# Performance work log

Measured on AMD Instinct MI355X. Metric: run time of the kernel, lower is better.

## Reference

```python
import jax, jax.numpy as jnp
import numpy as np

N, D = 320, 64


def setup_inputs() -> dict:
    key = jax.random.key(0)
    k1, k2, k3, k4, k5 = jax.random.split(key, 5)
    x = jax.random.normal(k1, (N, D), dtype=jnp.float32)
    sigma = jax.random.uniform(k2, (), dtype=jnp.float32) + 0.5  # positive scalar bandwidth
    score = jax.random.normal(k3, (N, D), dtype=jnp.float32)
    v = jax.random.normal(k4, (N, D), dtype=jnp.float32)
    grad_v_score = jax.random.normal(k5, (N, D), dtype=jnp.float32)
    return {"x": x, "sigma": sigma, "score": score, "v": v, "grad_v_score": grad_v_score}


def reference(x, sigma, score, v, grad_v_score):
    d = x.shape[-1]
    # od[i, j, :] = x_i - x_j   (torch: x.unsqueeze(-2) - x.unsqueeze(-3))
    od = x[:, None, :] - x[None, :, :]              # [N, N, D]
    ods = od * od                                    # [N, N, D]
    gamma = 1.0 / (sigma * sigma + 1e-8)             # scalar
    gods = gamma * ods                               # [N, N, D]
    k_d = jnp.exp(-0.5 * gods)                       # [N, N, D]
    k = k_d.mean(-1)                                 # [N, N]
    k_xj = gamma * k_d * od / d                      # [N, N, D]
    k_xi = -k_xj                                     # [N, N, D]
    tr_k_xj_xi = (gamma * (1.0 - gods) * k_d).mean(-1)  # [N, N]

    # score^T k_xk_xi k_xi term: ((1-gods) * score_j * k_xi * gamma) @ k_d^T / D  -> [N, N, N]
    A = (1.0 - gods) * score[None, :, :] * k_xi * gamma  # [N, N, D]
    score_t_k_xk_xi_k_xi = jnp.einsum('ijd,ikd->ijk', A, k_d) / d  # [N, N, N]

    # tr(k_xj_xi^T k_xk_xi) term -> [N, N, N]
    dot = jnp.einsum('ijd,ikd->ijk', od, od)         # (x_i-x_j).(x_i-x_k)
    t1 = dot * dot * (4.0 * gamma * gamma)
    sq = ods.sum(-1)                                  # pairwise squared distance [N, N]
    t2 = -2.0 * gamma * (sq[:, :, None] + sq[:, None, :])
    tr_k_xj_xi_t_k_xk_xi = (t1 + t2 + d) * k[:, :, None] * k[:, None, :] * (4.0 * gamma * gamma)

    # v^T k_xj_xi grad_v_score term -> [N, N]
    a = jnp.einsum('id,ijd->ij', v, od)              # v_i . (x_i - x_j)
    b = jnp.einsum('id,ijd->ij', grad_v_score, od)   # gvs_i . (x_i - x_j)
    vdot = (v * grad_v_score).sum(-1)[:, None]       # [N, 1]
    v_t_k_xj_xi_grad_v_score = (-2.0 * gamma * a * b + vdot) * k * (2.0 * gamma)

    return (k, k_xj, k_xi, tr_k_xj_xi, score_t_k_xk_xi_k_xi,
            tr_k_xj_xi_t_k_xk_xi, v_t_k_xj_xi_grad_v_score)
```

## Files before the change

### kernel.cpp

```cpp
#include <hip/hip_runtime.h>

#define N 320
#define D 64

__global__ __launch_bounds__(256) void pair_kernel(
    const float* __restrict__ x, const float* __restrict__ sigma,
    const float* __restrict__ score, const float* __restrict__ v,
    const float* __restrict__ gvs,
    float* __restrict__ out_k, float* __restrict__ out_kxj,
    float* __restrict__ out_kxi, float* __restrict__ out_tr,
    float* __restrict__ out_vt,
    float* __restrict__ wsA, float* __restrict__ wsK,
    float* __restrict__ wsSQ, float* __restrict__ wsG)
{
    int lane = threadIdx.x & 63;
    int p = blockIdx.x * 4 + (threadIdx.x >> 6);
    int i = p / N;
    int j = p - i * N;

    float sg = sigma[0];
    float gamma = 1.0f / (sg * sg + 1e-8f);

    float xi = x[i * D + lane];
    float xj = x[j * D + lane];
    float od = xi - xj;
    float ods = od * od;
    float gods = gamma * ods;
    float kd = __expf(-0.5f * gods);

    float kxj = gamma * kd * od * (1.0f / D);
    size_t pd = (size_t)p * D + lane;
    out_kxj[pd] = kxj;
    out_kxi[pd] = -kxj;

    float sj = score[j * D + lane];
    float Aval = (1.0f - gods) * sj * (-kxj) * gamma;
    wsA[pd] = Aval;
    wsK[pd] = kd;

    float vi = v[i * D + lane];
    float gi = gvs[i * D + lane];

    float r0 = kd;
    float r1 = gamma * (1.0f - gods) * kd;
    float r2 = ods;
    float r3 = vi * od;
    float r4 = gi * od;
    float r5 = vi * gi;
    float r6 = xi * xj;

    #pragma unroll
    for (int off = 32; off > 0; off >>= 1) {
        r0 += __shfl_xor(r0, off, 64);
        r1 += __shfl_xor(r1, off, 64);
        r2 += __shfl_xor(r2, off, 64);
        r3 += __shfl_xor(r3, off, 64);
        r4 += __shfl_xor(r4, off, 64);
        r5 += __shfl_xor(r5, off, 64);
        r6 += __shfl_xor(r6, off, 64);
    }

    if (lane == 0) {
        float kmean = r0 * (1.0f / D);
        out_k[p]  = kmean;
        out_tr[p] = r1 * (1.0f / D);
        wsSQ[p]   = r2;
        wsG[p]    = r6;
        out_vt[p] = (-2.0f * gamma * r3 * r4 + r5) * kmean * 2.0f * gamma;
    }
}

__global__ __launch_bounds__(N) void t6_kernel(
    const float* __restrict__ sigma,
    const float* __restrict__ k, const float* __restrict__ wsSQ,
    const float* __restrict__ wsG, float* __restrict__ out6)
{
    int kk = threadIdx.x;
    int j = blockIdx.x;
    int i = blockIdx.y;

    float sg = sigma[0];
    float gamma = 1.0f / (sg * sg + 1e-8f);
    float g2 = 4.0f * gamma * gamma;

    float Gii  = wsG[i * N + i];
    float Gij  = wsG[i * N + j];
    float kij  = k[i * N + j];
    float sqij = wsSQ[i * N + j];

    float Gjk  = wsG[j * N + kk];
    float Gik  = wsG[i * N + kk];
    float kik  = k[i * N + kk];
    float sqik = wsSQ[i * N + kk];

    float dot = Gii - Gij - Gik + Gjk;
    float t1 = dot * dot * g2;
    float t2 = -2.0f * gamma * (sqij + sqik);
    out6[((size_t)i * N + j) * N + kk] = (t1 + t2 + (float)D) * kij * kik * g2;
}

__global__ __launch_bounds__(256) void s5_kernel(
    const float* __restrict__ wsA, const float* __restrict__ wsK,
    float* __restrict__ out5)
{
    __shared__ float Alds[64 * 64];
    __shared__ float Klds[64 * 64];

    int i   = blockIdx.z;
    int j0  = blockIdx.y * 64;
    int kk0 = blockIdx.x * 64;
    int tid = threadIdx.x;

    int cw = tid & 15, rw = tid >> 4;
    const float* Abase = wsA + (size_t)(i * N + j0) * D;
    const float* Kbase = wsK + (size_t)(i * N + kk0) * D;
    #pragma unroll
    for (int q = 0; q < 4; ++q) {
        int r = rw + 16 * q;
        float4 av = *(const float4*)(Abase + r * D + cw * 4);
        float4 kv = *(const float4*)(Kbase + r * D + cw * 4);
        int sc = ((cw ^ (r & 7)) << 2);
        *(float4*)&Alds[r * 64 + sc] = av;
        *(float4*)&Klds[r * 64 + sc] = kv;
    }
    __syncthreads();

    int tk = tid & 15, tj = tid >> 4;
    float acc[4][4];
    #pragma unroll
    for (int a = 0; a < 4; ++a)
        #pragma unroll
        for (int b = 0; b < 4; ++b) acc[a][b] = 0.0f;

    #pragma unroll
    for (int c = 0; c < 16; ++c) {
        float4 a4[4], k4[4];
        #pragma unroll
        for (int jj = 0; jj < 4; ++jj) {
            int r = tj + 16 * jj;
            a4[jj] = *(const float4*)&Alds[r * 64 + ((c ^ (r & 7)) << 2)];
        }
        #pragma unroll
        for (int kki = 0; kki < 4; ++kki) {
            int r = tk + 16 * kki;
            k4[kki] = *(const float4*)&Klds[r * 64 + ((c ^ (r & 7)) << 2)];
        }
        #pragma unroll
        for (int jj = 0; jj < 4; ++jj)
            #pragma unroll
            for (int kki = 0; kki < 4; ++kki)
                acc[jj][kki] += a4[jj].x * k4[kki].x + a4[jj].y * k4[kki].y
                              + a4[jj].z * k4[kki].z + a4[jj].w * k4[kki].w;
    }

    #pragma unroll
    for (int jj = 0; jj < 4; ++jj) {
        int j = j0 + tj + 16 * jj;
        #pragma unroll
        for (int kki = 0; kki < 4; ++kki) {
            int kk = kk0 + tk + 16 * kki;
            out5[((size_t)i * N + j) * N + kk] = acc[jj][kki] * (1.0f / D);
        }
    }
}

extern "C" void kernel_launch(void* const* d_in, const int* in_sizes, int n_in,
                              void* d_out, int out_size, void* d_ws, size_t ws_size,
                              hipStream_t stream) {
    const float* x     = (const float*)d_in[0];
    const float* sigma = (const float*)d_in[1];
    const float* score = (const float*)d_in[2];
    const float* v     = (const float*)d_in[3];
    const float* gvs   = (const float*)d_in[4];

    float* out = (float*)d_out;
    float* out_k   = out;
    float* out_kxj = out + 102400;
    float* out_kxi = out + 6656000;
    float* out_tr  = out + 13209600;
    float* out5    = out + 13312000;
    float* out6    = out + 46080000;
    float* out_vt  = out + 78848000;

    float* ws   = (float*)d_ws;
    float* wsA  = ws;
    float* wsK  = ws + 6553600;
    float* wsSQ = ws + 13107200;
    float* wsG  = ws + 13209600;

    pair_kernel<<<dim3(N * N / 4), dim3(256), 0, stream>>>(
        x, sigma, score, v, gvs,
        out_k, out_kxj, out_kxi, out_tr, out_vt, wsA, wsK, wsSQ, wsG);

    t6_kernel<<<dim3(N, N), dim3(N), 0, stream>>>(sigma, out_k, wsSQ, wsG, out6);

    s5_kernel<<<dim3(5, 5, N), dim3(256), 0, stream>>>(wsA, wsK, out5);
}
```

Baseline: 429.6 us.

## Fuse t6 into s5 tile kernel and recompute A/K tiles on the fly

Removes the wsA/wsK workspace tensors. The triple kernel now recomputes the A and k_d tiles from x and score directly in its LDS load phase, and writes the out6 term in the same block that writes out5. The pair kernel is also restructured so each thread handles four elements with float4 loads and stores, using 16-lane reductions. This cuts roughly 50 MB of workspace write and read traffic and one kernel launch, at the cost of redundant exp computations per tile and scattered output stores for out6.

```diff
diff --git a/kernel.cpp b/kernel.cpp
--- a/kernel.cpp
+++ b/kernel.cpp
@@ -10,47 +10,56 @@
     float* __restrict__ out_k, float* __restrict__ out_kxj,
     float* __restrict__ out_kxi, float* __restrict__ out_tr,
     float* __restrict__ out_vt,
-    float* __restrict__ wsA, float* __restrict__ wsK,
     float* __restrict__ wsSQ, float* __restrict__ wsG)
 {
-    int lane = threadIdx.x & 63;
-    int p = blockIdx.x * 4 + (threadIdx.x >> 6);
+    int tid = threadIdx.x;
+    int sub = tid & 15;
+    int p = blockIdx.x * 16 + (tid >> 4);
     int i = p / N;
     int j = p - i * N;
 
     float sg = sigma[0];
     float gamma = 1.0f / (sg * sg + 1e-8f);
 
-    float xi = x[i * D + lane];
-    float xj = x[j * D + lane];
-    float od = xi - xj;
-    float ods = od * od;
-    float gods = gamma * ods;
-    float kd = __expf(-0.5f * gods);
-
-    float kxj = gamma * kd * od * (1.0f / D);
-    size_t pd = (size_t)p * D + lane;
-    out_kxj[pd] = kxj;
-    out_kxi[pd] = -kxj;
-
-    float sj = score[j * D + lane];
-    float Aval = (1.0f - gods) * sj * (-kxj) * gamma;
-    wsA[pd] = Aval;
-    wsK[pd] = kd;
-
-    float vi = v[i * D + lane];
-    float gi = gvs[i * D + lane];
-
-    float r0 = kd;
-    float r1 = gamma * (1.0f - gods) * kd;
-    float r2 = ods;
-    float r3 = vi * od;
-    float r4 = gi * od;
-    float r5 = vi * gi;
-    float r6 = xi * xj;
-
-    #pragma unroll
-    for (int off = 32; off > 0; off >>= 1) {
+    float4 xi4 = *(const float4*)(x     + i * D + sub * 4);
+    float4 xj4 = *(const float4*)(x     + j * D + sub * 4);
+    float4 sj4 = *(const float4*)(score + j * D + sub * 4);
+    float4 vi4 = *(const float4*)(v     + i * D + sub * 4);
+    float4 gi4 = *(const float4*)(gvs   + i * D + sub * 4);
+    const float* xi = (const float*)&xi4;
+    const float* xj = (const float*)&xj4;
+    const float* vi = (const float*)&vi4;
+    const float* gi = (const float*)&gi4;
+
+    float4 kxj4, kxi4;
+    float* kxjp = (float*)&kxj4;
+    float* kxip = (float*)&kxi4;
+
+    float r0 = 0.f, r1 = 0.f, r2 = 0.f, r3 = 0.f, r4 = 0.f, r5 = 0.f, r6 = 0.f;
+    #pragma unroll
+    for (int c = 0; c < 4; ++c) {
+        float od   = xi[c] - xj[c];
+        float ods  = od * od;
+        float gods = gamma * ods;
+        float kd   = __expf(-0.5f * gods);
+        float kxj  = gamma * kd * od * (1.0f / D);
+        kxjp[c] = kxj;
+        kxip[c] = -kxj;
+        r0 += kd;
+        r1 += gamma * (1.0f - gods) * kd;
+        r2 += ods;
+        r3 += vi[c] * od;
+        r4 += gi[c] * od;
+        r5 += vi[c] * gi[c];
+        r6 += xi[c] * xj[c];
+    }
+
+    size_t pd = (size_t)p * D + sub * 4;
+    *(float4*)(out_kxj + pd) = kxj4;
+    *(float4*)(out_kxi + pd) = kxi4;
+
+    #pragma unroll
+    for (int off = 8; off > 0; off >>= 1) {
         r0 += __shfl_xor(r0, off, 64);
         r1 += __shfl_xor(r1, off, 64);
         r2 += __shfl_xor(r2, off, 64);
@@ -60,7 +69,7 @@
         r6 += __shfl_xor(r6, off, 64);
     }
 
-    if (lane == 0) {
+    if (sub == 0) {
         float kmean = r0 * (1.0f / D);
         out_k[p]  = kmean;
         out_tr[p] = r1 * (1.0f / D);
@@ -70,38 +79,12 @@
     }
 }
 
-__global__ __launch_bounds__(N) void t6_kernel(
-    const float* __restrict__ sigma,
-    const float* __restrict__ k, const float* __restrict__ wsSQ,
-    const float* __restrict__ wsG, float* __restrict__ out6)
-{
-    int kk = threadIdx.x;
-    int j = blockIdx.x;
-    int i = blockIdx.y;
-
-    float sg = sigma[0];
-    float gamma = 1.0f / (sg * sg + 1e-8f);
-    float g2 = 4.0f * gamma * gamma;
-
-    float Gii  = wsG[i * N + i];
-    float Gij  = wsG[i * N + j];
-    float kij  = k[i * N + j];
-    float sqij = wsSQ[i * N + j];
-
-    float Gjk  = wsG[j * N + kk];
-    float Gik  = wsG[i * N + kk];
-    float kik  = k[i * N + kk];
-    float sqik = wsSQ[i * N + kk];
-
-    float dot = Gii - Gij - Gik + Gjk;
-    float t1 = dot * dot * g2;
-    float t2 = -2.0f * gamma * (sqij + sqik);
-    out6[((size_t)i * N + j) * N + kk] = (t1 + t2 + (float)D) * kij * kik * g2;
-}
-
-__global__ __launch_bounds__(256) void s5_kernel(
-    const float* __restrict__ wsA, const float* __restrict__ wsK,
-    float* __restrict__ out5)
+__global__ __launch_bounds__(256) void triple_kernel(
+    const float* __restrict__ x, const float* __restrict__ sigma,
+    const float* __restrict__ score,
+    const float* __restrict__ kmat, const float* __restrict__ wsSQ,
+    const float* __restrict__ wsG,
+    float* __restrict__ out5, float* __restrict__ out6)
 {
     __shared__ float Alds[64 * 64];
     __shared__ float Klds[64 * 64];
@@ -111,14 +94,35 @@
     int kk0 = blockIdx.x * 64;
     int tid = threadIdx.x;
 
+    float sg = sigma[0];
+    float gamma = 1.0f / (sg * sg + 1e-8f);
+    float cA = -gamma * gamma * (1.0f / D);
+    float g2 = 4.0f * gamma * gamma;
+
     int cw = tid & 15, rw = tid >> 4;
-    const float* Abase = wsA + (size_t)(i * N + j0) * D;
-    const float* Kbase = wsK + (size_t)(i * N + kk0) * D;
+    float4 xi4 = *(const float4*)(x + i * D + cw * 4);
+    const float* xi = (const float*)&xi4;
     #pragma unroll
     for (int q = 0; q < 4; ++q) {
         int r = rw + 16 * q;
-        float4 av = *(const float4*)(Abase + r * D + cw * 4);
-        float4 kv = *(const float4*)(Kbase + r * D + cw * 4);
+        float4 xj4 = *(const float4*)(x     + (j0  + r) * D + cw * 4);
+        float4 sj4 = *(const float4*)(score + (j0  + r) * D + cw * 4);
+        float4 xk4 = *(const float4*)(x     + (kk0 + r) * D + cw * 4);
+        const float* xj = (const float*)&xj4;
+        const float* sj = (const float*)&sj4;
+        const float* xk = (const float*)&xk4;
+        float4 av, kv;
+        float* avp = (float*)&av;
+        float* kvp = (float*)&kv;
+        #pragma unroll
+        for (int c = 0; c < 4; ++c) {
+            float odA  = xi[c] - xj[c];
+            float odsA = odA * odA;
+            float kdA  = __expf(-0.5f * gamma * odsA);
+            avp[c] = cA * (1.0f - gamma * odsA) * sj[c] * kdA * odA;
+            float odK = xi[c] - xk[c];
+            kvp[c] = __expf(-0.5f * gamma * odK * odK);
+        }
         int sc = ((cw ^ (r & 7)) << 2);
         *(float4*)&Alds[r * 64 + sc] = av;
         *(float4*)&Klds[r * 64 + sc] = kv;
@@ -153,13 +157,31 @@
                               + a4[jj].z * k4[kki].z + a4[jj].w * k4[kki].w;
     }
 
+    float Gii = wsG[i * N + i];
+    float kikv[4], sqikv[4], Gikv[4];
+    #pragma unroll
+    for (int kki = 0; kki < 4; ++kki) {
+        int kk = kk0 + tk + 16 * kki;
+        kikv[kki]  = kmat[i * N + kk];
+        sqikv[kki] = wsSQ[i * N + kk];
+        Gikv[kki]  = wsG[i * N + kk];
+    }
     #pragma unroll
     for (int jj = 0; jj < 4; ++jj) {
         int j = j0 + tj + 16 * jj;
+        float kij  = kmat[i * N + j];
+        float sqij = wsSQ[i * N + j];
+        float Gij  = wsG[i * N + j];
+        size_t rowbase = ((size_t)i * N + j) * N;
         #pragma unroll
         for (int kki = 0; kki < 4; ++kki) {
             int kk = kk0 + tk + 16 * kki;
-            out5[((size_t)i * N + j) * N + kk] = acc[jj][kki] * (1.0f / D);
+            out5[rowbase + kk] = acc[jj][kki] * (1.0f / D);
+            float Gjk = wsG[j * N + kk];
+            float dot = Gii - Gij - Gikv[kki] + Gjk;
+            float t1 = dot * dot * g2;
+            float t2 = -2.0f * gamma * (sqij + sqikv[kki]);
+            out6[rowbase + kk] = (t1 + t2 + (float)D) * kij * kikv[kki] * g2;
         }
     }
 }
@@ -183,16 +205,13 @@
     float* out_vt  = out + 78848000;
 
     float* ws   = (float*)d_ws;
-    float* wsA  = ws;
-    float* wsK  = ws + 6553600;
-    float* wsSQ = ws + 13107200;
-    float* wsG  = ws + 13209600;
-
-    pair_kernel<<<dim3(N * N / 4), dim3(256), 0, stream>>>(
+    float* wsSQ = ws;
+    float* wsG  = ws + 102400;
+
+    pair_kernel<<<dim3(N * N / 16), dim3(256), 0, stream>>>(
         x, sigma, score, v, gvs,
-        out_k, out_kxj, out_kxi, out_tr, out_vt, wsA, wsK, wsSQ, wsG);
-
-    t6_kernel<<<dim3(N, N), dim3(N), 0, stream>>>(sigma, out_k, wsSQ, wsG, out6);
-
-    s5_kernel<<<dim3(5, 5, N), dim3(256), 0, stream>>>(wsA, wsK, out5);
+        out_k, out_kxj, out_kxi, out_tr, out_vt, wsSQ, wsG);
+
+    triple_kernel<<<dim3(5, 5, N), dim3(256), 0, stream>>>(
+        x, sigma, score, out_k, wsSQ, wsG, out5, out6);
 }
```

After: 367.5 us. 1.17x faster.
